# Performance work log

Measured on AMD Instinct MI355X. Metric: run time of the kernel, lower is better.

Reference implementation:

```python
import jax, jax.numpy as jnp
import numpy as np
import math

D_MODEL = 1024
HEADS = 16
DK = D_MODEL // HEADS
SEQ = 4096
BATCH = 4
SCALE_BASE = 512.0
ROPE_BASE = 10000.0
GN_EPS = 1e-5


def _xpos(x):
    # x: [B, S, D]; RetNet-style xpos rotary with per-dim magnitude scale
    B, S, D = x.shape
    half = D // 2
    sv = (jnp.arange(0, D, 2, dtype=jnp.float32) + 0.4 * D) / (1.4 * D)      # [half]
    pos = jnp.arange(S, dtype=jnp.float32)
    scale = sv[None, :] ** (pos[:, None] / SCALE_BASE)                        # [S, half]
    inv_freq = 1.0 / (ROPE_BASE ** (jnp.arange(half, dtype=jnp.float32) / half))
    ang = pos[:, None] * inv_freq[None, :]                                    # [S, half]
    sin = jnp.repeat(jnp.sin(ang) * scale, 2, axis=-1)                        # [S, D] (duplicate_interleave)
    cos = jnp.repeat(jnp.cos(ang) * scale, 2, axis=-1)
    x1, x2 = x[..., ::2], x[..., 1::2]
    rot = jnp.stack((-x2, x1), axis=-1).reshape(x.shape)                      # rotate_every_two
    return x * cos[None] + rot * sin[None]


def _decay_D():
    # D[h, n, m] = gamma_h**(n-m) * (n >= m); n over d_k rows, m over seq cols
    gammas = 1.0 - jnp.exp(jnp.linspace(math.log(1.0 / 32), math.log(1.0 / 512), HEADS))
    n = jnp.arange(DK)[:, None]
    m = jnp.arange(SEQ)[None, :]
    mask = n >= m
    diff = jnp.maximum(n - m, 0).astype(jnp.float32)                          # avoid inf for n<m
    return jnp.where(mask[None], gammas[:, None, None] ** diff[None], 0.0)    # [H, DK, SEQ]


def _group_norm(y, gn_w, gn_b):
    # torch GroupNorm(HEADS, DK) applied to rows of length DK
    B, S, D = y.shape
    g = DK // HEADS
    z = y.reshape(-1, HEADS, g)
    mu = z.mean(axis=-1, keepdims=True)
    var = z.var(axis=-1, keepdims=True)
    z = (z - mu) * jax.lax.rsqrt(var + GN_EPS)
    z = z * gn_w.reshape(HEADS, g) + gn_b.reshape(HEADS, g)
    return z.reshape(B, S, D)


def setup_inputs():
    key = jax.random.key(0)
    ks = jax.random.split(key, 9)
    s_d = 1.0 / math.sqrt(D_MODEL)
    s_s = 1.0 / math.sqrt(SEQ)
    return {
        "q": jax.random.normal(ks[0], (BATCH, SEQ, D_MODEL), jnp.float32),
        "k": jax.random.normal(ks[1], (BATCH, SEQ, D_MODEL), jnp.float32),
        "v": jax.random.normal(ks[2], (BATCH, SEQ, D_MODEL), jnp.float32),
        "wq": jax.random.normal(ks[3], (D_MODEL, D_MODEL), jnp.float32) * s_d,
        "wk": jax.random.normal(ks[4], (D_MODEL, D_MODEL), jnp.float32) * s_d,
        "wv": jax.random.normal(ks[5], (D_MODEL, D_MODEL), jnp.float32) * s_d,
        "wo": jax.random.normal(ks[6], (D_MODEL, D_MODEL), jnp.float32) * s_d,
        "wg": jax.random.normal(ks[7], (D_MODEL, D_MODEL), jnp.float32) * s_d,
        "wx_w": jax.random.normal(ks[8], (DK, SEQ), jnp.float32) * s_s,
        "wx_b": jnp.zeros((DK,), jnp.float32),
        "gn_w": jnp.ones((DK,), jnp.float32),
        "gn_b": jnp.zeros((DK,), jnp.float32),
    }


def reference(q, k, v, wq, wk, wv, wo, wg, wx_w, wx_b, gn_w, gn_b):
    B, S, D = q.shape
    query = _xpos(q @ wq.T)
    keyx = _xpos(k @ wk.T)
    value = v @ wv.T
    qh = query.reshape(B, S, HEADS, DK).transpose(0, 2, 1, 3)   # [B,H,S,DK]
    kh = keyx.reshape(B, S, HEADS, DK).transpose(0, 2, 1, 3)
    vh = value.reshape(B, S, HEADS, DK).transpose(0, 2, 1, 3)
    # Linformer-style learnable projection over sequence: [B,H,DK,S] -> [B,H,DK,DK]
    kp = jnp.einsum('bhsd,es->bhde', kh, wx_w) + wx_b
    vp = jnp.einsum('bhsd,es->bhde', vh, wx_w) + wx_b
    Dt = _decay_D().transpose(0, 2, 1)                           # [H, S, DK]
    scores = jnp.einsum('bhsd,bhde->bhse', qh, kp) * Dt[None]    # [B,H,S,DK]
    attn = jax.nn.softmax(scores, axis=-1)
    y = jnp.einsum('bhse,bhfe->bhsf', attn, vp)                  # attn @ Vp^T -> [B,H,S,DK]
    y = y.transpose(0, 2, 1, 3).reshape(B, S, D)
    y = _group_norm(y, gn_w, gn_b)
    gate = (q @ wg.T) * y
    return (gate * jax.nn.sigmoid(gate)) @ wo.T
```

## Files before the change

kernel.cpp:

```cpp
#include <hip/hip_runtime.h>
#include <hip/hip_bf16.h>

#define DEVI __device__ __forceinline__

typedef __attribute__((ext_vector_type(8))) short  short8;
typedef __attribute__((ext_vector_type(4))) float  floatx4;
typedef __attribute__((ext_vector_type(8))) __bf16 bf16x8;

DEVI float b2f(unsigned short u){ union{unsigned int i; float f;} x; x.i=((unsigned int)u)<<16; return x.f; }
DEVI unsigned short f2b(float f){
  union{float ff; unsigned int i;} x; x.ff=f;
  unsigned int r = x.i + 0x7fffu + ((x.i>>16)&1u);
  return (unsigned short)(r>>16);
}

DEVI void lds_dma16(const void* g, void* l){
  __builtin_amdgcn_global_load_lds((const __attribute__((address_space(1))) void*)g,
                                   (__attribute__((address_space(3))) void*)l, 16, 0, 0);
}

DEVI floatx4 mfma_bf16(short8 a, short8 b, floatx4 c){
  return __builtin_amdgcn_mfma_f32_16x16x32_bf16(
      __builtin_bit_cast(bf16x8, a), __builtin_bit_cast(bf16x8, b), c, 0, 0, 0);
}

DEVI void tile_remap(long& bmi, long& bni){
  const int bx = blockIdx.x, by = blockIdx.y;
  if (gridDim.y == 128){
    bni = (long)(by & 7);
    bmi = (long)((bx << 4) + (by >> 3));
  } else {
    bni = bx; bmi = by;
  }
}


__global__ void cvt_kernel(const float* __restrict__ src, unsigned short* __restrict__ dst, int n8)
{
  const int i = blockIdx.x * 256 + threadIdx.x;
  if (i >= n8) return;
  floatx4 a = ((const floatx4*)src)[2*(size_t)i];
  floatx4 b = ((const floatx4*)src)[2*(size_t)i + 1];
  short8 o;
  o[0]=(short)f2b(a[0]); o[1]=(short)f2b(a[1]); o[2]=(short)f2b(a[2]); o[3]=(short)f2b(a[3]);
  o[4]=(short)f2b(b[0]); o[5]=(short)f2b(b[1]); o[6]=(short)f2b(b[2]); o[7]=(short)f2b(b[3]);
  *(short8*)&dst[(size_t)i*8] = o;
}

__global__ void cvt_split(const float* __restrict__ src, unsigned short* __restrict__ dh,
                          unsigned short* __restrict__ dl, int n8)
{
  const int i = blockIdx.x * 256 + threadIdx.x;
  if (i >= n8) return;
  floatx4 a = ((const floatx4*)src)[2*(size_t)i];
  floatx4 b = ((const floatx4*)src)[2*(size_t)i + 1];
  short8 h, l;
  #pragma unroll
  for (int j = 0; j < 8; j++){
    float x = (j < 4) ? a[j] : b[j-4];
    unsigned short hb = f2b(x);
    h[j] = (short)hb;
    l[j] = (short)f2b(x - b2f(hb));
  }
  *(short8*)&dh[(size_t)i*8] = h;
  *(short8*)&dl[(size_t)i*8] = l;
}

template<int GATE>
__global__ __launch_bounds__(256, 3)
void gemm_af32(const float* __restrict__ A, const unsigned short* __restrict__ Bw,
               unsigned short* __restrict__ C, int M, int N, int K,
               const float* __restrict__ zs, const float* __restrict__ zc)
{
  __shared__ __align__(16) short As[128*64];
  __shared__ __align__(16) short Bs[128*64];
  const int t    = threadIdx.x;
  const int lane = t & 63;
  const int w    = t >> 6, wm = w >> 1, wn = w & 1;
  const int l15  = lane & 15, kg = lane >> 4;
  const int sx   = (l15 & 7) * 8;
  long bmi, bni; tile_remap(bmi, bni);
  const long bm = bmi * 128, bn = bni * 128;

  const int sr = t >> 3, sc8 = (t & 7) * 8;
  const int scx = sc8 ^ ((sr & 7) * 8);
  const unsigned short* pb[4];
  const float* pa[4];
  short *lb[4], *la[4];
  #pragma unroll
  for (int u = 0; u < 4; u++){
    pb[u] = Bw + (bn + sr + u*32) * (size_t)K + scx;
    pa[u] = A  + (bm + sr + u*32) * (size_t)K + sc8;
    lb[u] = &Bs[(sr + u*32)*64 + sc8];
    la[u] = &As[(sr + u*32)*64 + scx];
  }

  floatx4 acc[4][4] = {};
  floatx4 cur[8], nxt[8];
  #pragma unroll
  for (int u = 0; u < 4; u++){
    cur[2*u]   = *(const floatx4*)(pa[u]);
    cur[2*u+1] = *(const floatx4*)(pa[u] + 4);
  }

  for (int k0 = 0; k0 < K; k0 += 64){
    __syncthreads();
    #pragma unroll
    for (int u = 0; u < 4; u++) lds_dma16(pb[u] + k0, lb[u]);
    #pragma unroll
    for (int u = 0; u < 4; u++){
      short8 h;
      #pragma unroll
      for (int j = 0; j < 8; j++){
        float x = (j < 4) ? cur[2*u][j] : cur[2*u+1][j-4];
        h[j] = (short)f2b(x);
      }
      *(short8*)la[u] = h;
    }
    __syncthreads();
    const int kn = (k0 + 64 < K) ? (k0 + 64) : k0;
    #pragma unroll
    for (int u = 0; u < 4; u++){
      nxt[2*u]   = *(const floatx4*)(pa[u] + kn);
      nxt[2*u+1] = *(const floatx4*)(pa[u] + kn + 4);
    }
    #pragma unroll
    for (int ks = 0; ks < 2; ks++){
      short8 af[4], bv[4];
      #pragma unroll
      for (int i = 0; i < 4; i++){
        af[i] = *(const short8*)&As[(wm*64 + i*16 + l15)*64 + ((ks*32 + kg*8) ^ sx)];
        bv[i] = *(const short8*)&Bs[(wn*64 + i*16 + l15)*64 + ((ks*32 + kg*8) ^ sx)];
      }
      #pragma unroll
      for (int i = 0; i < 4; i++)
        #pragma unroll
        for (int j = 0; j < 4; j++)
          acc[i][j] = mfma_bf16(af[i], bv[j], acc[i][j]);
    }
    #pragma unroll
    for (int r8 = 0; r8 < 8; r8++) cur[r8] = nxt[r8];
  }

  if (GATE){
    #pragma unroll
    for (int i = 0; i < 4; i++){
      const long mb = bm + wm*64 + i*16 + kg*4;
      #pragma unroll
      for (int r = 0; r < 4; r++){
        const long row = mb + r;
        const int  ss  = (int)(row & 4095);
        const long bb  = row >> 12;
        const float* zr = (ss < 64) ? (zs + (((size_t)(bb*64 + ss)) << 10))
                                    : (zc + ((size_t)bb << 10));
        #pragma unroll
        for (int j = 0; j < 4; j++){
          const long n = bn + wn*64 + j*16 + l15;
          float g = acc[i][j][r] * zr[n];
          float sig = 1.0f / (1.0f + __expf(-g));
          C[(size_t)row * N + n] = f2b(g * sig);
        }
      }
    }
  } else {
    #pragma unroll
    for (int i = 0; i < 4; i++){
      const long mb = bm + wm*64 + i*16 + kg*4;
      #pragma unroll
      for (int j = 0; j < 4; j++){
        const long n = bn + wn*64 + j*16 + l15;
        #pragma unroll
        for (int r = 0; r < 4; r++)
          C[(size_t)(mb + r) * N + n] = f2b(acc[i][j][r]);
      }
    }
  }
}

template<int QG>
__global__ __launch_bounds__(256, 2)
void gemm_split(const float* __restrict__ A, const unsigned short* __restrict__ Bh,
                const unsigned short* __restrict__ Bl, float* __restrict__ C,
                int M, int N, int K)
{
  __shared__ __align__(16) short Ash[128*64];
  __shared__ __align__(16) short Asl[128*64];
  __shared__ __align__(16) short Bsh[128*64];
  __shared__ __align__(16) short Bsl[128*64];
  const int t    = threadIdx.x;
  const int lane = t & 63;
  const int w    = t >> 6, wm = w >> 1, wn = w & 1;
  const int l15  = lane & 15, kg = lane >> 4;
  const int sx   = (l15 & 7) * 8;
  long bmi, bni; tile_remap(bmi, bni);
  const long bm = bmi * 128, bn = bni * 128;

  const int sr = t >> 3, sc8 = (t & 7) * 8;
  const int scx = sc8 ^ ((sr & 7) * 8);
  const unsigned short *pbh[4], *pbl[4];
  const float* pa[4];
  short *lbh[4], *lbl[4], *lah[4], *lal[4];
  #pragma unroll
  for (int u = 0; u < 4; u++){
    pbh[u] = Bh + (bn + sr + u*32) * (size_t)K + scx;
    pbl[u] = Bl + (bn + sr + u*32) * (size_t)K + scx;
    long ar = bm + sr + u*32;
    if (QG) ar = (ar >> 6) * 4096 + (ar & 63);
    pa[u]  = A + ar * (size_t)K + sc8;
    lbh[u] = &Bsh[(sr + u*32)*64 + sc8];
    lbl[u] = &Bsl[(sr + u*32)*64 + sc8];
    lah[u] = &Ash[(sr + u*32)*64 + scx];
    lal[u] = &Asl[(sr + u*32)*64 + scx];
  }

  floatx4 acc[4][4] = {};
  floatx4 cur[8], nxt[8];
  #pragma unroll
  for (int u = 0; u < 4; u++){
    cur[2*u]   = *(const floatx4*)(pa[u]);
    cur[2*u+1] = *(const floatx4*)(pa[u] + 4);
  }

  for (int k0 = 0; k0 < K; k0 += 64){
    __syncthreads();
    #pragma unroll
    for (int u = 0; u < 4; u++){
      lds_dma16(pbh[u] + k0, lbh[u]);
      lds_dma16(pbl[u] + k0, lbl[u]);
    }
    #pragma unroll
    for (int u = 0; u < 4; u++){
      short8 h, l;
      #pragma unroll
      for (int j = 0; j < 8; j++){
        float x = (j < 4) ? cur[2*u][j] : cur[2*u+1][j-4];
        unsigned short hb = f2b(x);
        h[j] = (short)hb;
        l[j] = (short)f2b(x - b2f(hb));
      }
      *(short8*)lah[u] = h;
      *(short8*)lal[u] = l;
    }
    __syncthreads();
    const int kn = (k0 + 64 < K) ? (k0 + 64) : k0;
    #pragma unroll
    for (int u = 0; u < 4; u++){
      nxt[2*u]   = *(const floatx4*)(pa[u] + kn);
      nxt[2*u+1] = *(const floatx4*)(pa[u] + kn + 4);
    }
    #pragma unroll
    for (int ks = 0; ks < 2; ks++){
      short8 afh[4], afl[4], bvh[4], bvl[4];
      #pragma unroll
      for (int i = 0; i < 4; i++){
        const int ro = (ks*32 + kg*8) ^ sx;
        afh[i] = *(const short8*)&Ash[(wm*64 + i*16 + l15)*64 + ro];
        afl[i] = *(const short8*)&Asl[(wm*64 + i*16 + l15)*64 + ro];
        bvh[i] = *(const short8*)&Bsh[(wn*64 + i*16 + l15)*64 + ro];
        bvl[i] = *(const short8*)&Bsl[(wn*64 + i*16 + l15)*64 + ro];
      }
      #pragma unroll
      for (int i = 0; i < 4; i++)
        #pragma unroll
        for (int j = 0; j < 4; j++){
          acc[i][j] = mfma_bf16(afh[i], bvh[j], acc[i][j]);
          acc[i][j] = mfma_bf16(afh[i], bvl[j], acc[i][j]);
          acc[i][j] = mfma_bf16(afl[i], bvh[j], acc[i][j]);
        }
    }
    #pragma unroll
    for (int r8 = 0; r8 < 8; r8++) cur[r8] = nxt[r8];
  }

  const int smask = QG ? 63 : 4095;
  #pragma unroll
  for (int j = 0; j < 4; j++){
    const long n  = bn + wn*64 + j*16 + l15;
    const int  ip = (int)(n >> 1);
    const float lsv  = __logf((2.0f*ip + 409.6f) * (1.0f/1433.6f));
    const float invf = __expf(-(float)ip * (9.2103403720f/512.0f));
    const float sgn  = (n & 1) ? 1.0f : -1.0f;
    #pragma unroll
    for (int i = 0; i < 4; i++){
      const long mb = bm + wm*64 + i*16 + kg*4;
      #pragma unroll
      for (int r = 0; r < 4; r++){
        float x = acc[i][j][r];
        float p = __shfl_xor(x, 1);
        const float fs = (float)((int)((mb + r) & smask));
        const float scale = __expf(lsv * fs * (1.0f/512.0f));
        float sn, cs;
        __sincosf(fs * invf, &sn, &cs);
        sn *= scale; cs *= scale;
        C[(size_t)(mb + r) * N + n] = x*cs + sgn*(p*sn);
      }
    }
  }
}

__global__ __launch_bounds__(256, 2)
void proj_split(const float* __restrict__ X0, const unsigned short* __restrict__ wxh,
                const unsigned short* __restrict__ wxl, float* __restrict__ P)
{
  __shared__ __align__(16) short Wsh[64*32];
  __shared__ __align__(16) short Wsl[64*32];
  __shared__ __align__(16) short Xth[64*40];
  __shared__ __align__(16) short Xtl[64*40];
  const int t = threadIdx.x, w = t >> 6, lane = t & 63;
  const int l15 = lane & 15, kg = lane >> 4;
  const int d0 = blockIdx.x * 64;
  const int b  = blockIdx.y;
  const float* X = X0 + (size_t)b * 4096 * 1024;
  const int s0 = blockIdx.z * 512;
  const int ssr = t >> 3, ddr = (t & 7) * 8;
  floatx4 acc[4] = {};

  for (int kk = 0; kk < 512; kk += 32){
    const int s = s0 + kk;
    floatx4 x0 = *(const floatx4*)&X[(size_t)(s + ssr) * 1024 + d0 + ddr];
    floatx4 x1 = *(const floatx4*)&X[(size_t)(s + ssr) * 1024 + d0 + ddr + 4];
    __syncthreads();
    lds_dma16(&wxh[(size_t)(t >> 2) * 4096 + s + (t & 3) * 8], &Wsh[t*8]);
    lds_dma16(&wxl[(size_t)(t >> 2) * 4096 + s + (t & 3) * 8], &Wsl[t*8]);
    float xv[8] = {x0[0],x0[1],x0[2],x0[3],x1[0],x1[1],x1[2],x1[3]};
    #pragma unroll
    for (int j = 0; j < 8; j++){
      unsigned short hb = f2b(xv[j]);
      Xth[(ddr + j) * 40 + ssr] = (short)hb;
      Xtl[(ddr + j) * 40 + ssr] = (short)f2b(xv[j] - b2f(hb));
    }
    __syncthreads();
    short8 afh = *(const short8*)&Wsh[(w*16 + l15)*32 + kg*8];
    short8 afl = *(const short8*)&Wsl[(w*16 + l15)*32 + kg*8];
    #pragma unroll
    for (int j = 0; j < 4; j++){
      short8 bvh = *(const short8*)&Xth[(j*16 + l15)*40 + kg*8];
      short8 bvl = *(const short8*)&Xtl[(j*16 + l15)*40 + kg*8];
      acc[j] = mfma_bf16(afh, bvh, acc[j]);
      acc[j] = mfma_bf16(afh, bvl, acc[j]);
      acc[j] = mfma_bf16(afl, bvh, acc[j]);
    }
  }
  float* Pb = P + (size_t)(b*2) * 65536;
  #pragma unroll
  for (int j = 0; j < 4; j++)
    #pragma unroll
    for (int r = 0; r < 4; r++)
      atomicAdd(&Pb[(w*16 + kg*4 + r) * 1024 + d0 + j*16 + l15], acc[j][r]);
}

__global__ __launch_bounds__(256, 2)
void proj_bf16(const unsigned short* __restrict__ X0, const unsigned short* __restrict__ wxw_bf,
               float* __restrict__ P)
{
  __shared__ __align__(16) short Ws[64*32];
  __shared__ __align__(16) short Xt[64*40];
  const int t = threadIdx.x, w = t >> 6, lane = t & 63;
  const int l15 = lane & 15, kg = lane >> 4;
  const int d0 = blockIdx.x * 64;
  const int b  = blockIdx.y;
  const unsigned short* X = X0 + (size_t)b * 4096 * 1024;
  const int s0 = blockIdx.z * 512;
  const int ssr = t >> 3, ddr = (t & 7) * 8;
  floatx4 acc[4] = {};

  for (int kk = 0; kk < 512; kk += 32){
    const int s = s0 + kk;
    short8 xv = *(const short8*)&X[(size_t)(s + ssr) * 1024 + d0 + ddr];
    __syncthreads();
    lds_dma16(&wxw_bf[(size_t)(t >> 2) * 4096 + s + (t & 3) * 8], &Ws[t*8]);
    #pragma unroll
    for (int j = 0; j < 8; j++) Xt[(ddr + j) * 40 + ssr] = xv[j];
    __syncthreads();
    short8 af = *(const short8*)&Ws[(w*16 + l15)*32 + kg*8];
    #pragma unroll
    for (int j = 0; j < 4; j++){
      short8 bv = *(const short8*)&Xt[(j*16 + l15)*40 + kg*8];
      acc[j] = mfma_bf16(af, bv, acc[j]);
    }
  }
  float* Pb = P + (size_t)(b*2 + 1) * 65536;
  #pragma unroll
  for (int j = 0; j < 4; j++)
    #pragma unroll
    for (int r = 0; r < 4; r++)
      atomicAdd(&Pb[(w*16 + kg*4 + r) * 1024 + d0 + j*16 + l15], acc[j][r]);
}

__global__ __launch_bounds__(256)
void attn_kernel(const float* __restrict__ P, const float* __restrict__ Qx,
                 const float* __restrict__ wxb,
                 const float* __restrict__ gnw, const float* __restrict__ gnb,
                 float* __restrict__ zs, float* __restrict__ zc)
{
  __shared__ __align__(16) float kps[64*64];
  __shared__ __align__(16) float vps[64*64];
  __shared__ __align__(16) float scs[64*65];
  __shared__ float pm[256];
  __shared__ float ym[64];
  const int t = threadIdx.x;
  const int w = t >> 6, s = t & 63;
  const int b = blockIdx.x >> 4, h = blockIdx.x & 15;
  const float* Pk = P + (size_t)(2*b) * 65536 + h*64;
  const float* Pv = Pk + 65536;

  {
    const int e = t >> 2, c = (t & 3) * 16;
    const float wb = wxb[e];
    #pragma unroll
    for (int j = 0; j < 4; j++){
      floatx4 kv = *(const floatx4*)&Pk[(size_t)e*1024 + c + 4*j];
      floatx4 vv = *(const floatx4*)&Pv[(size_t)e*1024 + c + 4*j];
      kv.x += wb; kv.y += wb; kv.z += wb; kv.w += wb;
      vv.x += wb; vv.y += wb; vv.z += wb; vv.w += wb;
      *(floatx4*)&kps[e*64 + c + 4*j] = kv;
      *(floatx4*)&vps[e*64 + c + 4*j] = vv;
    }
  }
  __syncthreads();

  float qf[64];
  const floatx4* q4 = (const floatx4*)(Qx + (size_t)(b*64 + s)*1024 + h*64);
  #pragma unroll
  for (int i = 0; i < 16; i++){
    floatx4 qq = q4[i];
    qf[4*i] = qq.x; qf[4*i+1] = qq.y; qf[4*i+2] = qq.z; qf[4*i+3] = qq.w;
  }

  #pragma unroll
  for (int eo = 0; eo < 16; eo++){
    const int e = w*16 + eo;
    const floatx4* kp4 = (const floatx4*)&kps[e*64];
    float dot = 0.f;
    #pragma unroll
    for (int d = 0; d < 16; d++){
      floatx4 kv = kp4[d];
      dot += qf[4*d]*kv.x + qf[4*d+1]*kv.y + qf[4*d+2]*kv.z + qf[4*d+3]*kv.w;
    }
    scs[e*65 + s] = dot;
  }
  {
    float am = 0.f;
    #pragma unroll
    for (int eo = 0; eo < 16; eo++) am += vps[(w*16 + eo)*64 + s];
    pm[t] = am;
  }
  __syncthreads();

  const float lg = -3.4657359028f - 0.1848392483f * (float)h;
  const float gamma = 1.0f - __expf(lg);
  float sc[64];
  #pragma unroll
  for (int e = 0; e < 64; e++) sc[e] = scs[e*65 + s];
  float dec = 1.0f;
  #pragma unroll
  for (int e = 0; e < 64; e++){
    bool on = (e >= s);
    sc[e] = on ? sc[e]*dec : 0.0f;
    if (on) dec *= gamma;
  }
  float mx = -1e30f;
  #pragma unroll
  for (int e = 0; e < 64; e++) mx = fmaxf(mx, sc[e]);
  float Z = 0.f;
  #pragma unroll
  for (int e = 0; e < 64; e++){ sc[e] = __expf(sc[e] - mx); Z += sc[e]; }
  const float rz = 1.0f / Z;

  #pragma unroll
  for (int go = 0; go < 4; go++){
    const int g = w*4 + go;
    floatx4 y = {0.f,0.f,0.f,0.f};
    #pragma unroll
    for (int e = 0; e < 64; e++){
      floatx4 vv = *(const floatx4*)&vps[e*64 + g*4];
      y += sc[e] * vv;
    }
    y *= rz;
    float mu = (y.x + y.y + y.z + y.w) * 0.25f;
    float a0 = y.x-mu, a1 = y.y-mu, a2 = y.z-mu, a3 = y.w-mu;
    float inv = rsqrtf((a0*a0 + a1*a1 + a2*a2 + a3*a3)*0.25f + 1e-5f);
    floatx4 o;
    o.x = a0*inv*gnw[g*4+0] + gnb[g*4+0];
    o.y = a1*inv*gnw[g*4+1] + gnb[g*4+1];
    o.z = a2*inv*gnw[g*4+2] + gnb[g*4+2];
    o.w = a3*inv*gnw[g*4+3] + gnb[g*4+3];
    *(floatx4*)&zs[(size_t)(b*64 + s)*1024 + h*64 + g*4] = o;
  }

  if (w == 0)
    ym[s] = (pm[s] + pm[64+s] + pm[128+s] + pm[192+s]) * (1.0f/64.0f);
  __syncthreads();
  if (t < 16){
    float a0 = ym[t*4], a1 = ym[t*4+1], a2 = ym[t*4+2], a3 = ym[t*4+3];
    float mu = (a0+a1+a2+a3)*0.25f;
    a0 -= mu; a1 -= mu; a2 -= mu; a3 -= mu;
    float inv = rsqrtf((a0*a0+a1*a1+a2*a2+a3*a3)*0.25f + 1e-5f);
    zc[(size_t)b*1024 + h*64 + t*4+0] = a0*inv*gnw[t*4+0] + gnb[t*4+0];
    zc[(size_t)b*1024 + h*64 + t*4+1] = a1*inv*gnw[t*4+1] + gnb[t*4+1];
    zc[(size_t)b*1024 + h*64 + t*4+2] = a2*inv*gnw[t*4+2] + gnb[t*4+2];
    zc[(size_t)b*1024 + h*64 + t*4+3] = a3*inv*gnw[t*4+3] + gnb[t*4+3];
  }
}

__global__ __launch_bounds__(256, 3)
void gemm_bt(const unsigned short* __restrict__ A, const unsigned short* __restrict__ Bw,
             float* __restrict__ C, int M, int N, int K)
{
  __shared__ __align__(16) short As[128*64];
  __shared__ __align__(16) short Bs[128*64];
  const int t    = threadIdx.x;
  const int lane = t & 63;
  const int w    = t >> 6, wm = w >> 1, wn = w & 1;
  const int l15  = lane & 15, kg = lane >> 4;
  const int sx   = (l15 & 7) * 8;
  long bmi, bni; tile_remap(bmi, bni);
  const long bm = bmi * 128, bn = bni * 128;

  const int sr = t >> 3, sc8 = (t & 7) * 8;
  const int scx = sc8 ^ ((sr & 7) * 8);
  const unsigned short *pa[4], *pb[4];
  short *la[4], *lb[4];
  #pragma unroll
  for (int u = 0; u < 4; u++){
    pa[u] = A  + (bm + sr + u*32) * (size_t)K + scx;
    pb[u] = Bw + (bn + sr + u*32) * (size_t)K + scx;
    la[u] = &As[(sr + u*32)*64 + sc8];
    lb[u] = &Bs[(sr + u*32)*64 + sc8];
  }

  floatx4 acc[4][4] = {};

  for (int k0 = 0; k0 < K; k0 += 64){
    __syncthreads();
    #pragma unroll
    for (int u = 0; u < 4; u++){
      lds_dma16(pa[u] + k0, la[u]);
      lds_dma16(pb[u] + k0, lb[u]);
    }
    __syncthreads();
    #pragma unroll
    for (int ks = 0; ks < 2; ks++){
      short8 af[4], bv[4];
      #pragma unroll
      for (int i = 0; i < 4; i++){
        af[i] = *(const short8*)&As[(wm*64 + i*16 + l15)*64 + ((ks*32 + kg*8) ^ sx)];
        bv[i] = *(const short8*)&Bs[(wn*64 + i*16 + l15)*64 + ((ks*32 + kg*8) ^ sx)];
      }
      #pragma unroll
      for (int i = 0; i < 4; i++)
        #pragma unroll
        for (int j = 0; j < 4; j++)
          acc[i][j] = mfma_bf16(af[i], bv[j], acc[i][j]);
    }
  }

  #pragma unroll
  for (int i = 0; i < 4; i++){
    const long mb = bm + wm*64 + i*16 + kg*4;
    #pragma unroll
    for (int j = 0; j < 4; j++){
      const long n = bn + wn*64 + j*16 + l15;
      #pragma unroll
      for (int r = 0; r < 4; r++)
        C[(size_t)(mb + r) * N + n] = acc[i][j][r];
    }
  }
}

extern "C" void kernel_launch(void* const* d_in, const int* in_sizes, int n_in,
                              void* d_out, int out_size, void* d_ws, size_t ws_size,
                              hipStream_t stream)
{
  const float* q   = (const float*)d_in[0];
  const float* k   = (const float*)d_in[1];
  const float* v   = (const float*)d_in[2];
  const float* wq  = (const float*)d_in[3];
  const float* wk  = (const float*)d_in[4];
  const float* wv  = (const float*)d_in[5];
  const float* wo  = (const float*)d_in[6];
  const float* wg  = (const float*)d_in[7];
  const float* wxw = (const float*)d_in[8];
  const float* wxb = (const float*)d_in[9];
  const float* gnw = (const float*)d_in[10];
  const float* gnb = (const float*)d_in[11];

  char* ws = (char*)d_ws;
  unsigned short* A0   = (unsigned short*)(ws);
  unsigned short* wh   = (unsigned short*)(ws + 33554432);
  unsigned short* wl   = (unsigned short*)(ws + 35651584);
  unsigned short* wAbf = (unsigned short*)(ws + 37748736);
  unsigned short* wgbf = (unsigned short*)(ws + 39845888);
  unsigned short* wxh  = (unsigned short*)(ws + 41943040);
  unsigned short* wxl  = (unsigned short*)(ws + 42467328);
  float*          P    = (float*)(ws + 42991616);
  float*          zs   = (float*)(ws + 45088768);
  float*          zc   = (float*)(ws + 46137344);
  float*          Qx   = (float*)(ws + 46153728);
  float*          Kx   = (float*)d_out;

  const int M = 16384, N = 1024, K = 1024;
  dim3 blk(256);

  cvt_split<<<512, blk, 0, stream>>>(wk, wh, wl, 131072);
  cvt_split<<<128, blk, 0, stream>>>(wxw, wxh, wxl, 32768);
  cvt_kernel<<<512, blk, 0, stream>>>(wv, wAbf, 131072);
  cvt_kernel<<<512, blk, 0, stream>>>(wg, wgbf, 131072);
  hipMemsetAsync(P, 0, 2097152, stream);

  gemm_split<0><<<dim3(8,128), blk, 0, stream>>>(k, wh, wl, Kx, M, N, K);
  proj_split<<<dim3(16,4,8), blk, 0, stream>>>(Kx, wxh, wxl, P);

  gemm_af32<0><<<dim3(8,128), blk, 0, stream>>>(v, wAbf, A0, M, N, K, nullptr, nullptr);
  proj_bf16<<<dim3(16,4,8), blk, 0, stream>>>(A0, wxh, P);
  cvt_kernel<<<512, blk, 0, stream>>>(wo, wAbf, 131072);

  cvt_split<<<512, blk, 0, stream>>>(wq, wh, wl, 131072);
  gemm_split<1><<<dim3(8,2), blk, 0, stream>>>(q, wh, wl, Qx, 256, N, K);
  attn_kernel<<<64, 256, 0, stream>>>(P, Qx, wxb, gnw, gnb, zs, zc);

  gemm_af32<1><<<dim3(8,128), blk, 0, stream>>>(q, wgbf, A0, M, N, K, zs, zc);
  gemm_bt<<<dim3(8,128), blk, 0, stream>>>(A0, wAbf, (float*)d_out, M, N, K);
}
```

Baseline: 593.6 us.

## Double-buffer LDS with 32-wide K tiles in all GEMM kernels

```diff
diff --git a/kernel.cpp b/kernel.cpp
--- a/kernel.cpp
+++ b/kernel.cpp
@@ -72,74 +72,83 @@
                unsigned short* __restrict__ C, int M, int N, int K,
                const float* __restrict__ zs, const float* __restrict__ zc)
 {
-  __shared__ __align__(16) short As[128*64];
-  __shared__ __align__(16) short Bs[128*64];
+  __shared__ __align__(16) short As[2][128*32];
+  __shared__ __align__(16) short Bs[2][128*32];
   const int t    = threadIdx.x;
   const int lane = t & 63;
   const int w    = t >> 6, wm = w >> 1, wn = w & 1;
   const int l15  = lane & 15, kg = lane >> 4;
-  const int sx   = (l15 & 7) * 8;
+  const int sxr  = ((l15 >> 1) & 3) * 8;
   long bmi, bni; tile_remap(bmi, bni);
   const long bm = bmi * 128, bn = bni * 128;
 
-  const int sr = t >> 3, sc8 = (t & 7) * 8;
-  const int scx = sc8 ^ ((sr & 7) * 8);
-  const unsigned short* pb[4];
-  const float* pa[4];
-  short *lb[4], *la[4];
-  #pragma unroll
-  for (int u = 0; u < 4; u++){
-    pb[u] = Bw + (bn + sr + u*32) * (size_t)K + scx;
-    pa[u] = A  + (bm + sr + u*32) * (size_t)K + sc8;
-    lb[u] = &Bs[(sr + u*32)*64 + sc8];
-    la[u] = &As[(sr + u*32)*64 + scx];
-  }
+  size_t bgo[2]; int bls[2];
+  #pragma unroll
+  for (int u = 0; u < 2; u++){
+    const int cl  = u*256 + t;
+    const int row = cl >> 2, cr = cl & 3;
+    const int csrc = cr ^ ((row >> 1) & 3);
+    bgo[u] = (size_t)(bn + row) * K + csrc*8;
+    bls[u] = cl * 8;
+  }
+  const int arow = t >> 1, acolb = (t & 1) * 16;
+  const float* pa = A + (bm + arow) * (size_t)K + acolb;
+  const int aw0 = arow*32 + ((((t&1)*2    ) ^ ((t>>2)&3)))*8;
+  const int aw1 = arow*32 + ((((t&1)*2 + 1) ^ ((t>>2)&3)))*8;
 
   floatx4 acc[4][4] = {};
-  floatx4 cur[8], nxt[8];
-  #pragma unroll
-  for (int u = 0; u < 4; u++){
-    cur[2*u]   = *(const floatx4*)(pa[u]);
-    cur[2*u+1] = *(const floatx4*)(pa[u] + 4);
-  }
-
-  for (int k0 = 0; k0 < K; k0 += 64){
+  floatx4 sta[4], stb[4];
+
+  #pragma unroll
+  for (int u = 0; u < 2; u++) lds_dma16(Bw + bgo[u], &Bs[0][bls[u]]);
+  #pragma unroll
+  for (int u = 0; u < 4; u++) sta[u] = *(const floatx4*)(pa + u*4);
+  {
+    short8 h0, h1;
+    #pragma unroll
+    for (int j = 0; j < 8; j++){
+      h0[j] = (short)f2b(sta[j>>2][j&3]);
+      h1[j] = (short)f2b(sta[2 + (j>>2)][j&3]);
+    }
+    *(short8*)&As[0][aw0] = h0; *(short8*)&As[0][aw1] = h1;
+  }
+  #pragma unroll
+  for (int u = 0; u < 4; u++) sta[u] = *(const floatx4*)(pa + 32 + u*4);
+  __syncthreads();
+
+  const int NT = K >> 5;
+  int o = 0;
+  for (int kt = 0; kt < NT; ++kt){
+    if (kt + 1 < NT){
+      short8 h0, h1;
+      #pragma unroll
+      for (int j = 0; j < 8; j++){
+        h0[j] = (short)f2b(sta[j>>2][j&3]);
+        h1[j] = (short)f2b(sta[2 + (j>>2)][j&3]);
+      }
+      *(short8*)&As[o^1][aw0] = h0; *(short8*)&As[o^1][aw1] = h1;
+      const int k1 = (kt + 1) << 5;
+      #pragma unroll
+      for (int u = 0; u < 2; u++) lds_dma16(Bw + bgo[u] + k1, &Bs[o^1][bls[u]]);
+      const int k2 = ((kt + 2 < NT) ? (kt + 2) : kt) << 5;
+      #pragma unroll
+      for (int u = 0; u < 4; u++) stb[u] = *(const floatx4*)(pa + k2 + u*4);
+    }
+    short8 af[4], bv[4];
+    #pragma unroll
+    for (int i = 0; i < 4; i++){
+      af[i] = *(const short8*)&As[o][(wm*64 + i*16 + l15)*32 + ((kg*8) ^ sxr)];
+      bv[i] = *(const short8*)&Bs[o][(wn*64 + i*16 + l15)*32 + ((kg*8) ^ sxr)];
+    }
+    #pragma unroll
+    for (int i = 0; i < 4; i++)
+      #pragma unroll
+      for (int j = 0; j < 4; j++)
+        acc[i][j] = mfma_bf16(af[i], bv[j], acc[i][j]);
     __syncthreads();
-    #pragma unroll
-    for (int u = 0; u < 4; u++) lds_dma16(pb[u] + k0, lb[u]);
-    #pragma unroll
-    for (int u = 0; u < 4; u++){
-      short8 h;
-      #pragma unroll
-      for (int j = 0; j < 8; j++){
-        float x = (j < 4) ? cur[2*u][j] : cur[2*u+1][j-4];
-        h[j] = (short)f2b(x);
-      }
-      *(short8*)la[u] = h;
-    }
-    __syncthreads();
-    const int kn = (k0 + 64 < K) ? (k0 + 64) : k0;
-    #pragma unroll
-    for (int u = 0; u < 4; u++){
-      nxt[2*u]   = *(const floatx4*)(pa[u] + kn);
-      nxt[2*u+1] = *(const floatx4*)(pa[u] + kn + 4);
-    }
-    #pragma unroll
-    for (int ks = 0; ks < 2; ks++){
-      short8 af[4], bv[4];
-      #pragma unroll
-      for (int i = 0; i < 4; i++){
-        af[i] = *(const short8*)&As[(wm*64 + i*16 + l15)*64 + ((ks*32 + kg*8) ^ sx)];
-        bv[i] = *(const short8*)&Bs[(wn*64 + i*16 + l15)*64 + ((ks*32 + kg*8) ^ sx)];
-      }
-      #pragma unroll
-      for (int i = 0; i < 4; i++)
-        #pragma unroll
-        for (int j = 0; j < 4; j++)
-          acc[i][j] = mfma_bf16(af[i], bv[j], acc[i][j]);
-    }
-    #pragma unroll
-    for (int r8 = 0; r8 < 8; r8++) cur[r8] = nxt[r8];
+    o ^= 1;
+    #pragma unroll
+    for (int u = 0; u < 4; u++) sta[u] = stb[u];
   }
 
   if (GATE){
@@ -183,93 +192,106 @@
                 const unsigned short* __restrict__ Bl, float* __restrict__ C,
                 int M, int N, int K)
 {
-  __shared__ __align__(16) short Ash[128*64];
-  __shared__ __align__(16) short Asl[128*64];
-  __shared__ __align__(16) short Bsh[128*64];
-  __shared__ __align__(16) short Bsl[128*64];
+  __shared__ __align__(16) short Ash[2][128*32];
+  __shared__ __align__(16) short Asl[2][128*32];
+  __shared__ __align__(16) short Bsh[2][128*32];
+  __shared__ __align__(16) short Bsl[2][128*32];
   const int t    = threadIdx.x;
   const int lane = t & 63;
   const int w    = t >> 6, wm = w >> 1, wn = w & 1;
   const int l15  = lane & 15, kg = lane >> 4;
-  const int sx   = (l15 & 7) * 8;
+  const int sxr  = ((l15 >> 1) & 3) * 8;
   long bmi, bni; tile_remap(bmi, bni);
   const long bm = bmi * 128, bn = bni * 128;
 
-  const int sr = t >> 3, sc8 = (t & 7) * 8;
-  const int scx = sc8 ^ ((sr & 7) * 8);
-  const unsigned short *pbh[4], *pbl[4];
-  const float* pa[4];
-  short *lbh[4], *lbl[4], *lah[4], *lal[4];
-  #pragma unroll
-  for (int u = 0; u < 4; u++){
-    pbh[u] = Bh + (bn + sr + u*32) * (size_t)K + scx;
-    pbl[u] = Bl + (bn + sr + u*32) * (size_t)K + scx;
-    long ar = bm + sr + u*32;
-    if (QG) ar = (ar >> 6) * 4096 + (ar & 63);
-    pa[u]  = A + ar * (size_t)K + sc8;
-    lbh[u] = &Bsh[(sr + u*32)*64 + sc8];
-    lbl[u] = &Bsl[(sr + u*32)*64 + sc8];
-    lah[u] = &Ash[(sr + u*32)*64 + scx];
-    lal[u] = &Asl[(sr + u*32)*64 + scx];
-  }
+  size_t bgo[2]; int bls[2];
+  #pragma unroll
+  for (int u = 0; u < 2; u++){
+    const int cl  = u*256 + t;
+    const int row = cl >> 2, cr = cl & 3;
+    const int csrc = cr ^ ((row >> 1) & 3);
+    bgo[u] = (size_t)(bn + row) * K + csrc*8;
+    bls[u] = cl * 8;
+  }
+  const int arow = t >> 1, acolb = (t & 1) * 16;
+  long ar = bm + arow;
+  if (QG) ar = (ar >> 6) * 4096 + (ar & 63);
+  const float* pa = A + ar * (size_t)K + acolb;
+  const int aw0 = arow*32 + ((((t&1)*2    ) ^ ((t>>2)&3)))*8;
+  const int aw1 = arow*32 + ((((t&1)*2 + 1) ^ ((t>>2)&3)))*8;
 
   floatx4 acc[4][4] = {};
-  floatx4 cur[8], nxt[8];
-  #pragma unroll
-  for (int u = 0; u < 4; u++){
-    cur[2*u]   = *(const floatx4*)(pa[u]);
-    cur[2*u+1] = *(const floatx4*)(pa[u] + 4);
-  }
-
-  for (int k0 = 0; k0 < K; k0 += 64){
+  floatx4 sta[4], stb[4];
+
+  #pragma unroll
+  for (int u = 0; u < 2; u++){
+    lds_dma16(Bh + bgo[u], &Bsh[0][bls[u]]);
+    lds_dma16(Bl + bgo[u], &Bsl[0][bls[u]]);
+  }
+  #pragma unroll
+  for (int u = 0; u < 4; u++) sta[u] = *(const floatx4*)(pa + u*4);
+  {
+    short8 h0, h1, l0, l1;
+    #pragma unroll
+    for (int j = 0; j < 8; j++){
+      float x0 = sta[j>>2][j&3], x1 = sta[2 + (j>>2)][j&3];
+      unsigned short hb0 = f2b(x0), hb1 = f2b(x1);
+      h0[j] = (short)hb0; l0[j] = (short)f2b(x0 - b2f(hb0));
+      h1[j] = (short)hb1; l1[j] = (short)f2b(x1 - b2f(hb1));
+    }
+    *(short8*)&Ash[0][aw0] = h0; *(short8*)&Ash[0][aw1] = h1;
+    *(short8*)&Asl[0][aw0] = l0; *(short8*)&Asl[0][aw1] = l1;
+  }
+  #pragma unroll
+  for (int u = 0; u < 4; u++) sta[u] = *(const floatx4*)(pa + 32 + u*4);
+  __syncthreads();
+
+  const int NT = K >> 5;
+  int o = 0;
+  for (int kt = 0; kt < NT; ++kt){
+    if (kt + 1 < NT){
+      short8 h0, h1, l0, l1;
+      #pragma unroll
+      for (int j = 0; j < 8; j++){
+        float x0 = sta[j>>2][j&3], x1 = sta[2 + (j>>2)][j&3];
+        unsigned short hb0 = f2b(x0), hb1 = f2b(x1);
+        h0[j] = (short)hb0; l0[j] = (short)f2b(x0 - b2f(hb0));
+        h1[j] = (short)hb1; l1[j] = (short)f2b(x1 - b2f(hb1));
+      }
+      *(short8*)&Ash[o^1][aw0] = h0; *(short8*)&Ash[o^1][aw1] = h1;
+      *(short8*)&Asl[o^1][aw0] = l0; *(short8*)&Asl[o^1][aw1] = l1;
+      const int k1 = (kt + 1) << 5;
+      #pragma unroll
+      for (int u = 0; u < 2; u++){
+        lds_dma16(Bh + bgo[u] + k1, &Bsh[o^1][bls[u]]);
+        lds_dma16(Bl + bgo[u] + k1, &Bsl[o^1][bls[u]]);
+      }
+      const int k2 = ((kt + 2 < NT) ? (kt + 2) : kt) << 5;
+      #pragma unroll
+      for (int u = 0; u < 4; u++) stb[u] = *(const floatx4*)(pa + k2 + u*4);
+    }
+    short8 afh[4], afl[4], bvh[4], bvl[4];
+    #pragma unroll
+    for (int i = 0; i < 4; i++){
+      const int ra = (wm*64 + i*16 + l15)*32 + ((kg*8) ^ sxr);
+      const int rb = (wn*64 + i*16 + l15)*32 + ((kg*8) ^ sxr);
+      afh[i] = *(const short8*)&Ash[o][ra];
+      afl[i] = *(const short8*)&Asl[o][ra];
+      bvh[i] = *(const short8*)&Bsh[o][rb];
+      bvl[i] = *(const short8*)&Bsl[o][rb];
+    }
+    #pragma unroll
+    for (int i = 0; i < 4; i++)
+      #pragma unroll
+      for (int j = 0; j < 4; j++){
+        acc[i][j] = mfma_bf16(afh[i], bvh[j], acc[i][j]);
+        acc[i][j] = mfma_bf16(afh[i], bvl[j], acc[i][j]);
+        acc[i][j] = mfma_bf16(afl[i], bvh[j], acc[i][j]);
+      }
     __syncthreads();
-    #pragma unroll
-    for (int u = 0; u < 4; u++){
-      lds_dma16(pbh[u] + k0, lbh[u]);
-      lds_dma16(pbl[u] + k0, lbl[u]);
-    }
-    #pragma unroll
-    for (int u = 0; u < 4; u++){
-      short8 h, l;
-      #pragma unroll
-      for (int j = 0; j < 8; j++){
-        float x = (j < 4) ? cur[2*u][j] : cur[2*u+1][j-4];
-        unsigned short hb = f2b(x);
-        h[j] = (short)hb;
-        l[j] = (short)f2b(x - b2f(hb));
-      }
-      *(short8*)lah[u] = h;
-      *(short8*)lal[u] = l;
-    }
-    __syncthreads();
-    const int kn = (k0 + 64 < K) ? (k0 + 64) : k0;
-    #pragma unroll
-    for (int u = 0; u < 4; u++){
-      nxt[2*u]   = *(const floatx4*)(pa[u] + kn);
-      nxt[2*u+1] = *(const floatx4*)(pa[u] + kn + 4);
-    }
-    #pragma unroll
-    for (int ks = 0; ks < 2; ks++){
-      short8 afh[4], afl[4], bvh[4], bvl[4];
-      #pragma unroll
-      for (int i = 0; i < 4; i++){
-        const int ro = (ks*32 + kg*8) ^ sx;
-        afh[i] = *(const short8*)&Ash[(wm*64 + i*16 + l15)*64 + ro];
-        afl[i] = *(const short8*)&Asl[(wm*64 + i*16 + l15)*64 + ro];
-        bvh[i] = *(const short8*)&Bsh[(wn*64 + i*16 + l15)*64 + ro];
-        bvl[i] = *(const short8*)&Bsl[(wn*64 + i*16 + l15)*64 + ro];
-      }
-      #pragma unroll
-      for (int i = 0; i < 4; i++)
-        #pragma unroll
-        for (int j = 0; j < 4; j++){
-          acc[i][j] = mfma_bf16(afh[i], bvh[j], acc[i][j]);
-          acc[i][j] = mfma_bf16(afh[i], bvl[j], acc[i][j]);
-          acc[i][j] = mfma_bf16(afl[i], bvh[j], acc[i][j]);
-        }
-    }
-    #pragma unroll
-    for (int r8 = 0; r8 < 8; r8++) cur[r8] = nxt[r8];
+    o ^= 1;
+    #pragma unroll
+    for (int u = 0; u < 4; u++) sta[u] = stb[u];
   }
 
   const int smask = QG ? 63 : 4095;
@@ -507,52 +529,60 @@
 void gemm_bt(const unsigned short* __restrict__ A, const unsigned short* __restrict__ Bw,
              float* __restrict__ C, int M, int N, int K)
 {
-  __shared__ __align__(16) short As[128*64];
-  __shared__ __align__(16) short Bs[128*64];
+  __shared__ __align__(16) short As[2][128*32];
+  __shared__ __align__(16) short Bs[2][128*32];
   const int t    = threadIdx.x;
   const int lane = t & 63;
   const int w    = t >> 6, wm = w >> 1, wn = w & 1;
   const int l15  = lane & 15, kg = lane >> 4;
-  const int sx   = (l15 & 7) * 8;
+  const int sxr  = ((l15 >> 1) & 3) * 8;
   long bmi, bni; tile_remap(bmi, bni);
   const long bm = bmi * 128, bn = bni * 128;
 
-  const int sr = t >> 3, sc8 = (t & 7) * 8;
-  const int scx = sc8 ^ ((sr & 7) * 8);
-  const unsigned short *pa[4], *pb[4];
-  short *la[4], *lb[4];
-  #pragma unroll
-  for (int u = 0; u < 4; u++){
-    pa[u] = A  + (bm + sr + u*32) * (size_t)K + scx;
-    pb[u] = Bw + (bn + sr + u*32) * (size_t)K + scx;
-    la[u] = &As[(sr + u*32)*64 + sc8];
-    lb[u] = &Bs[(sr + u*32)*64 + sc8];
+  size_t ago[2], bgo[2]; int bls[2];
+  #pragma unroll
+  for (int u = 0; u < 2; u++){
+    const int cl  = u*256 + t;
+    const int row = cl >> 2, cr = cl & 3;
+    const int csrc = cr ^ ((row >> 1) & 3);
+    ago[u] = (size_t)(bm + row) * K + csrc*8;
+    bgo[u] = (size_t)(bn + row) * K + csrc*8;
+    bls[u] = cl * 8;
   }
 
   floatx4 acc[4][4] = {};
 
-  for (int k0 = 0; k0 < K; k0 += 64){
+  #pragma unroll
+  for (int u = 0; u < 2; u++){
+    lds_dma16(A  + ago[u], &As[0][bls[u]]);
+    lds_dma16(Bw + bgo[u], &Bs[0][bls[u]]);
+  }
+  __syncthreads();
+
+  const int NT = K >> 5;
+  int o = 0;
+  for (int kt = 0; kt < NT; ++kt){
+    if (kt + 1 < NT){
+      const int k1 = (kt + 1) << 5;
+      #pragma unroll
+      for (int u = 0; u < 2; u++){
+        lds_dma16(A  + ago[u] + k1, &As[o^1][bls[u]]);
+        lds_dma16(Bw + bgo[u] + k1, &Bs[o^1][bls[u]]);
+      }
+    }
+    short8 af[4], bv[4];
+    #pragma unroll
+    for (int i = 0; i < 4; i++){
+      af[i] = *(const short8*)&As[o][(wm*64 + i*16 + l15)*32 + ((kg*8) ^ sxr)];
+      bv[i] = *(const short8*)&Bs[o][(wn*64 + i*16 + l15)*32 + ((kg*8) ^ sxr)];
+    }
+    #pragma unroll
+    for (int i = 0; i < 4; i++)
+      #pragma unroll
+      for (int j = 0; j < 4; j++)
+        acc[i][j] = mfma_bf16(af[i], bv[j], acc[i][j]);
     __syncthreads();
-    #pragma unroll
-    for (int u = 0; u < 4; u++){
-      lds_dma16(pa[u] + k0, la[u]);
-      lds_dma16(pb[u] + k0, lb[u]);
-    }
-    __syncthreads();
-    #pragma unroll
-    for (int ks = 0; ks < 2; ks++){
-      short8 af[4], bv[4];
-      #pragma unroll
-      for (int i = 0; i < 4; i++){
-        af[i] = *(const short8*)&As[(wm*64 + i*16 + l15)*64 + ((ks*32 + kg*8) ^ sx)];
-        bv[i] = *(const short8*)&Bs[(wn*64 + i*16 + l15)*64 + ((ks*32 + kg*8) ^ sx)];
-      }
-      #pragma unroll
-      for (int i = 0; i < 4; i++)
-        #pragma unroll
-        for (int j = 0; j < 4; j++)
-          acc[i][j] = mfma_bf16(af[i], bv[j], acc[i][j]);
-    }
+    o ^= 1;
   }
 
   #pragma unroll
```

Measured after the change: 634.3 us. +6.9%, slower.

## Prefetch next B tile via LDS DMA while computing current tile in GEMMs

Applied to the files above, without the earlier changes.

```diff
diff --git a/kernel.cpp b/kernel.cpp
--- a/kernel.cpp
+++ b/kernel.cpp
@@ -96,17 +96,18 @@
   }
 
   floatx4 acc[4][4] = {};
-  floatx4 cur[8], nxt[8];
+  floatx4 cur[8];
   #pragma unroll
   for (int u = 0; u < 4; u++){
     cur[2*u]   = *(const floatx4*)(pa[u]);
     cur[2*u+1] = *(const floatx4*)(pa[u] + 4);
   }
-
-  for (int k0 = 0; k0 < K; k0 += 64){
-    __syncthreads();
-    #pragma unroll
-    for (int u = 0; u < 4; u++) lds_dma16(pb[u] + k0, lb[u]);
+  #pragma unroll
+  for (int u = 0; u < 4; u++) lds_dma16(pb[u], lb[u]);
+
+  const int NT = K >> 6;
+  for (int kt = 0; kt < NT; ++kt){
+    __syncthreads();
     #pragma unroll
     for (int u = 0; u < 4; u++){
       short8 h;
@@ -117,29 +118,36 @@
       }
       *(short8*)la[u] = h;
     }
-    __syncthreads();
-    const int kn = (k0 + 64 < K) ? (k0 + 64) : k0;
+    short8 bv[2][4];
+    #pragma unroll
+    for (int ks = 0; ks < 2; ks++)
+      #pragma unroll
+      for (int i = 0; i < 4; i++)
+        bv[ks][i] = *(const short8*)&Bs[(wn*64 + i*16 + l15)*64 + ((ks*32 + kg*8) ^ sx)];
+    __syncthreads();
+    const int kn = (kt + 1 < NT) ? ((kt + 1) << 6) : 0;
+    if (kt + 1 < NT){
+      #pragma unroll
+      for (int u = 0; u < 4; u++) lds_dma16(pb[u] + kn, lb[u]);
+    }
     #pragma unroll
     for (int u = 0; u < 4; u++){
-      nxt[2*u]   = *(const floatx4*)(pa[u] + kn);
-      nxt[2*u+1] = *(const floatx4*)(pa[u] + kn + 4);
-    }
+      cur[2*u]   = *(const floatx4*)(pa[u] + kn);
+      cur[2*u+1] = *(const floatx4*)(pa[u] + kn + 4);
+    }
+    __builtin_amdgcn_sched_barrier(0);
     #pragma unroll
     for (int ks = 0; ks < 2; ks++){
-      short8 af[4], bv[4];
-      #pragma unroll
-      for (int i = 0; i < 4; i++){
+      short8 af[4];
+      #pragma unroll
+      for (int i = 0; i < 4; i++)
         af[i] = *(const short8*)&As[(wm*64 + i*16 + l15)*64 + ((ks*32 + kg*8) ^ sx)];
-        bv[i] = *(const short8*)&Bs[(wn*64 + i*16 + l15)*64 + ((ks*32 + kg*8) ^ sx)];
-      }
       #pragma unroll
       for (int i = 0; i < 4; i++)
         #pragma unroll
         for (int j = 0; j < 4; j++)
-          acc[i][j] = mfma_bf16(af[i], bv[j], acc[i][j]);
-    }
-    #pragma unroll
-    for (int r8 = 0; r8 < 8; r8++) cur[r8] = nxt[r8];
+          acc[i][j] = mfma_bf16(af[i], bv[ks][j], acc[i][j]);
+    }
   }
 
   if (GATE){
@@ -214,20 +222,21 @@
   }
 
   floatx4 acc[4][4] = {};
-  floatx4 cur[8], nxt[8];
+  floatx4 cur[8];
   #pragma unroll
   for (int u = 0; u < 4; u++){
     cur[2*u]   = *(const floatx4*)(pa[u]);
     cur[2*u+1] = *(const floatx4*)(pa[u] + 4);
   }
-
-  for (int k0 = 0; k0 < K; k0 += 64){
-    __syncthreads();
-    #pragma unroll
-    for (int u = 0; u < 4; u++){
-      lds_dma16(pbh[u] + k0, lbh[u]);
-      lds_dma16(pbl[u] + k0, lbl[u]);
-    }
+  #pragma unroll
+  for (int u = 0; u < 4; u++){
+    lds_dma16(pbh[u], lbh[u]);
+    lds_dma16(pbl[u], lbl[u]);
+  }
+
+  const int NT = K >> 6;
+  for (int kt = 0; kt < NT; ++kt){
+    __syncthreads();
     #pragma unroll
     for (int u = 0; u < 4; u++){
       short8 h, l;
@@ -241,35 +250,48 @@
       *(short8*)lah[u] = h;
       *(short8*)lal[u] = l;
     }
-    __syncthreads();
-    const int kn = (k0 + 64 < K) ? (k0 + 64) : k0;
+    short8 bvh[2][4], bvl[2][4];
+    #pragma unroll
+    for (int ks = 0; ks < 2; ks++)
+      #pragma unroll
+      for (int i = 0; i < 4; i++){
+        const int rb = (wn*64 + i*16 + l15)*64 + ((ks*32 + kg*8) ^ sx);
+        bvh[ks][i] = *(const short8*)&Bsh[rb];
+        bvl[ks][i] = *(const short8*)&Bsl[rb];
+      }
+    __syncthreads();
+    const int kn = (kt + 1 < NT) ? ((kt + 1) << 6) : 0;
+    if (kt + 1 < NT){
+      #pragma unroll
+      for (int u = 0; u < 4; u++){
+        lds_dma16(pbh[u] + kn, lbh[u]);
+        lds_dma16(pbl[u] + kn, lbl[u]);
+      }
+    }
     #pragma unroll
     for (int u = 0; u < 4; u++){
-      nxt[2*u]   = *(const floatx4*)(pa[u] + kn);
-      nxt[2*u+1] = *(const floatx4*)(pa[u] + kn + 4);
-    }
+      cur[2*u]   = *(const floatx4*)(pa[u] + kn);
+      cur[2*u+1] = *(const floatx4*)(pa[u] + kn + 4);
+    }
+    __builtin_amdgcn_sched_barrier(0);
     #pragma unroll
     for (int ks = 0; ks < 2; ks++){
-      short8 afh[4], afl[4], bvh[4], bvl[4];
+      short8 afh[4], afl[4];
       #pragma unroll
       for (int i = 0; i < 4; i++){
-        const int ro = (ks*32 + kg*8) ^ sx;
-        afh[i] = *(const short8*)&Ash[(wm*64 + i*16 + l15)*64 + ro];
-        afl[i] = *(const short8*)&Asl[(wm*64 + i*16 + l15)*64 + ro];
-        bvh[i] = *(const short8*)&Bsh[(wn*64 + i*16 + l15)*64 + ro];
-        bvl[i] = *(const short8*)&Bsl[(wn*64 + i*16 + l15)*64 + ro];
+        const int ra = (wm*64 + i*16 + l15)*64 + ((ks*32 + kg*8) ^ sx);
+        afh[i] = *(const short8*)&Ash[ra];
+        afl[i] = *(const short8*)&Asl[ra];
       }
       #pragma unroll
       for (int i = 0; i < 4; i++)
         #pragma unroll
         for (int j = 0; j < 4; j++){
-          acc[i][j] = mfma_bf16(afh[i], bvh[j], acc[i][j]);
-          acc[i][j] = mfma_bf16(afh[i], bvl[j], acc[i][j]);
-          acc[i][j] = mfma_bf16(afl[i], bvh[j], acc[i][j]);
+          acc[i][j] = mfma_bf16(afh[i], bvh[ks][j], acc[i][j]);
+          acc[i][j] = mfma_bf16(afh[i], bvl[ks][j], acc[i][j]);
+          acc[i][j] = mfma_bf16(afl[i], bvh[ks][j], acc[i][j]);
         }
     }
-    #pragma unroll
-    for (int r8 = 0; r8 < 8; r8++) cur[r8] = nxt[r8];
   }
 
   const int smask = QG ? 63 : 4095;
@@ -531,28 +553,40 @@
 
   floatx4 acc[4][4] = {};
 
-  for (int k0 = 0; k0 < K; k0 += 64){
-    __syncthreads();
-    #pragma unroll
-    for (int u = 0; u < 4; u++){
-      lds_dma16(pa[u] + k0, la[u]);
-      lds_dma16(pb[u] + k0, lb[u]);
-    }
-    __syncthreads();
-    #pragma unroll
-    for (int ks = 0; ks < 2; ks++){
-      short8 af[4], bv[4];
+  #pragma unroll
+  for (int u = 0; u < 4; u++){
+    lds_dma16(pa[u], la[u]);
+    lds_dma16(pb[u], lb[u]);
+  }
+
+  const int NT = K >> 6;
+  for (int kt = 0; kt < NT; ++kt){
+    __syncthreads();
+    short8 af[2][4], bv[2][4];
+    #pragma unroll
+    for (int ks = 0; ks < 2; ks++)
       #pragma unroll
       for (int i = 0; i < 4; i++){
-        af[i] = *(const short8*)&As[(wm*64 + i*16 + l15)*64 + ((ks*32 + kg*8) ^ sx)];
-        bv[i] = *(const short8*)&Bs[(wn*64 + i*16 + l15)*64 + ((ks*32 + kg*8) ^ sx)];
-      }
+        af[ks][i] = *(const short8*)&As[(wm*64 + i*16 + l15)*64 + ((ks*32 + kg*8) ^ sx)];
+        bv[ks][i] = *(const short8*)&Bs[(wn*64 + i*16 + l15)*64 + ((ks*32 + kg*8) ^ sx)];
+      }
+    __syncthreads();
+    if (kt + 1 < NT){
+      const int kn = (kt + 1) << 6;
+      #pragma unroll
+      for (int u = 0; u < 4; u++){
+        lds_dma16(pa[u] + kn, la[u]);
+        lds_dma16(pb[u] + kn, lb[u]);
+      }
+    }
+    __builtin_amdgcn_sched_barrier(0);
+    #pragma unroll
+    for (int ks = 0; ks < 2; ks++)
       #pragma unroll
       for (int i = 0; i < 4; i++)
         #pragma unroll
         for (int j = 0; j < 4; j++)
-          acc[i][j] = mfma_bf16(af[i], bv[j], acc[i][j]);
-    }
+          acc[i][j] = mfma_bf16(af[ks][i], bv[ks][j], acc[i][j]);
   }
 
   #pragma unroll
```

New measurement: 596.1 us. About the same (+0.4%).
